# Performance work log

Measured on AMD Instinct MI355X. Metric: run time of the kernel, lower is better.

The kernel has to match this reference:

```python
import jax, jax.numpy as jnp
import numpy as np

DM, NEXPERTS, SETS, ESIZE = 1024, 32, 4, 32
B, S = 2, 8192


def setup_inputs() -> dict:
    key = jax.random.key(0)
    ks = jax.random.split(key, 7)
    sc = 0.02
    return {
        "x": jax.random.normal(ks[0], (B, S, DM), jnp.float32),
        "Wc": jax.random.normal(ks[1], (DM, NEXPERTS, SETS), jnp.float32) * sc,
        "bc": jax.random.normal(ks[2], (NEXPERTS, SETS), jnp.float32) * sc,
        "W1": jax.random.normal(ks[3], (NEXPERTS, SETS, DM, ESIZE), jnp.float32) * sc,
        "b1": jax.random.normal(ks[4], (NEXPERTS, SETS, ESIZE), jnp.float32) * sc,
        "W2": jax.random.normal(ks[5], (NEXPERTS, SETS, DM, ESIZE), jnp.float32) * sc,
        "b2": jax.random.normal(ks[6], (NEXPERTS, SETS, DM), jnp.float32) * sc,
    }


def reference(x, Wc, bc, W1, b1, W2, b2):
    b, s, d = x.shape
    g = Wc.shape[1]          # nexperts (= tokens per group)
    # group tokens: [..., (n g), d] -> [..., n, g, d]
    grouped = x.reshape(b, s // g, g, d)
    # controller logits: [b, n, t, e, s]
    logits = jnp.einsum('bntd,des->bntes', grouped, Wc) + bc
    # tie-breaker varying along the token axis (dim -3)
    tie = jnp.linspace(0.0, 1e-6, g, dtype=x.dtype).reshape(-1, 1, 1)
    logits = logits + tie
    # hard one-hot permutation: argmax over tokens per (expert, set)
    perm = (logits == jnp.max(logits, axis=-3, keepdims=True)).astype(x.dtype)
    # dispatch: [b, n, e, s, d]
    permuted = jnp.einsum('bntd,bntes->bnesd', grouped, perm)
    # per-(expert,set) MLP
    inner = jax.nn.relu(jnp.einsum('bnesd,esdf->bnesf', permuted, W1) + b1)
    result_permuted = jnp.einsum('bnesf,esdf->bnesd', inner, W2) + b2
    # combine back to tokens: [b, n, t, d]
    result = jnp.einsum('bnesd,bntes->bntd', result_permuted, perm)
    return result.reshape(b, s, d)
```

## Files before the change

### kernel.cpp

```cpp
#include <hip/hip_runtime.h>
#include <hip/hip_bf16.h>

#define DM   1024
#define NES  128
#define GT   32
#define NGRP 512
#define FSZ  32
#define MARGIN_EPS 1e-3f

typedef float f32x4 __attribute__((ext_vector_type(4)));
typedef short s16x8 __attribute__((ext_vector_type(8)));

__device__ inline unsigned short f2bf(float f) {
  union { float f; unsigned int u; } x; x.f = f;
  unsigned int r = x.u + 0x7fffu + ((x.u >> 16) & 1u);
  return (unsigned short)(r >> 16);
}
__device__ inline float bf2f(unsigned short h) {
  union { unsigned int u; float f; } x; x.u = ((unsigned int)h) << 16;
  return x.f;
}

__global__ __launch_bounds__(256) void kSplit(const float* __restrict__ x,
                                              unsigned short* __restrict__ xh,
                                              unsigned short* __restrict__ xl) {
  size_t i = ((size_t)blockIdx.x * 256 + threadIdx.x) * 8;
  float4 a = *(const float4*)&x[i];
  float4 b = *(const float4*)&x[i + 4];
  float v[8] = {a.x, a.y, a.z, a.w, b.x, b.y, b.z, b.w};
  s16x8 h, lo;
#pragma unroll
  for (int k = 0; k < 8; ++k) {
    unsigned short hh = f2bf(v[k]);
    h[k]  = (short)hh;
    lo[k] = (short)f2bf(v[k] - bf2f(hh));
  }
  *(s16x8*)&xh[i] = h;
  *(s16x8*)&xl[i] = lo;
}

__global__ __launch_bounds__(256) void kW(const float* __restrict__ W1,
                                          const float* __restrict__ W2,
                                          const float* __restrict__ Wc,
                                          unsigned short* __restrict__ W1f,
                                          unsigned short* __restrict__ W2f,
                                          unsigned short* __restrict__ Wchf,
                                          unsigned short* __restrict__ Wclf) {
  const int bid = blockIdx.x;
  if (bid < 2048) {
    int idx = bid * 256 + threadIdx.x;
    int l = idx & 63, nh = (idx >> 6) & 1, kt = (idx >> 7) & 31, es = idx >> 12;
    const float* src = W1 + ((size_t)es * DM + kt * 32 + (l >> 4) * 8) * FSZ
                          + nh * 16 + (l & 15);
    s16x8 v;
#pragma unroll
    for (int i = 0; i < 8; ++i) v[i] = (short)f2bf(src[(size_t)i * FSZ]);
    *(s16x8*)(W1f + (size_t)idx * 8) = v;
  } else if (bid < 4096) {
    int idx = (bid - 2048) * 256 + threadIdx.x;
    int l = idx & 63, dt = (idx >> 6) & 63, es = idx >> 12;
    const float* src = W2 + ((size_t)es * DM + dt * 16 + (l & 15)) * FSZ + (l >> 4) * 8;
    float4 a = *(const float4*)src;
    float4 b = *(const float4*)(src + 4);
    s16x8 v;
    v[0] = (short)f2bf(a.x); v[1] = (short)f2bf(a.y);
    v[2] = (short)f2bf(a.z); v[3] = (short)f2bf(a.w);
    v[4] = (short)f2bf(b.x); v[5] = (short)f2bf(b.y);
    v[6] = (short)f2bf(b.z); v[7] = (short)f2bf(b.w);
    *(s16x8*)(W2f + (size_t)idx * 8) = v;
  } else {
    int idx = (bid - 4096) * 256 + threadIdx.x;
    int l = idx & 63, nt = (idx >> 6) & 7, kt = idx >> 9;
    const float* src = Wc + (size_t)(kt * 32 + (l >> 4) * 8) * NES + nt * 16 + (l & 15);
    s16x8 h, lo;
#pragma unroll
    for (int i = 0; i < 8; ++i) {
      float v = src[(size_t)i * NES];
      unsigned short hh = f2bf(v);
      h[i]  = (short)hh;
      lo[i] = (short)f2bf(v - bf2f(hh));
    }
    *(s16x8*)(Wchf + (size_t)idx * 8) = h;
    *(s16x8*)(Wclf + (size_t)idx * 8) = lo;
  }
}

__global__ __launch_bounds__(256, 2) void kLg(const unsigned short* __restrict__ xh,
                                              const unsigned short* __restrict__ xl,
                                              const unsigned short* __restrict__ Wchf,
                                              const unsigned short* __restrict__ Wclf,
                                              const float* __restrict__ bc,
                                              unsigned int* __restrict__ sel,
                                              unsigned int* __restrict__ flags,
                                              unsigned int* __restrict__ cnt) {
  __shared__ float lg[GT * NES];
  const int g   = blockIdx.x;
  const int tid = threadIdx.x;
  const int l   = tid & 63, w = tid >> 6;
  const int r15 = l & 15, q = l >> 4;

  const unsigned short* ah0 = xh + ((size_t)g * GT + r15) * DM + q * 8;
  const unsigned short* ah1 = ah0 + 16 * DM;
  const unsigned short* al0 = xl + ((size_t)g * GT + r15) * DM + q * 8;
  const unsigned short* al1 = al0 + 16 * DM;

  f32x4 acc[2][2];
#pragma unroll
  for (int i = 0; i < 2; ++i)
#pragma unroll
    for (int j = 0; j < 2; ++j) acc[i][j] = (f32x4){0.f, 0.f, 0.f, 0.f};

  for (int kt = 0; kt < 32; ++kt) {
    s16x8 Ah0 = *(const s16x8*)(ah0 + kt * 32);
    s16x8 Ah1 = *(const s16x8*)(ah1 + kt * 32);
    s16x8 Al0 = *(const s16x8*)(al0 + kt * 32);
    s16x8 Al1 = *(const s16x8*)(al1 + kt * 32);
    const size_t boff = (((size_t)kt * 8 + w * 2) * 64 + l) * 8;
    s16x8 Bh0 = *(const s16x8*)(Wchf + boff);
    s16x8 Bh1 = *(const s16x8*)(Wchf + boff + 64 * 8);
    s16x8 Bl0 = *(const s16x8*)(Wclf + boff);
    s16x8 Bl1 = *(const s16x8*)(Wclf + boff + 64 * 8);
    acc[0][0] = __builtin_amdgcn_mfma_f32_16x16x32_bf16(Ah0, Bh0, acc[0][0], 0, 0, 0);
    acc[0][0] = __builtin_amdgcn_mfma_f32_16x16x32_bf16(Al0, Bh0, acc[0][0], 0, 0, 0);
    acc[0][0] = __builtin_amdgcn_mfma_f32_16x16x32_bf16(Ah0, Bl0, acc[0][0], 0, 0, 0);
    acc[0][1] = __builtin_amdgcn_mfma_f32_16x16x32_bf16(Ah0, Bh1, acc[0][1], 0, 0, 0);
    acc[0][1] = __builtin_amdgcn_mfma_f32_16x16x32_bf16(Al0, Bh1, acc[0][1], 0, 0, 0);
    acc[0][1] = __builtin_amdgcn_mfma_f32_16x16x32_bf16(Ah0, Bl1, acc[0][1], 0, 0, 0);
    acc[1][0] = __builtin_amdgcn_mfma_f32_16x16x32_bf16(Ah1, Bh0, acc[1][0], 0, 0, 0);
    acc[1][0] = __builtin_amdgcn_mfma_f32_16x16x32_bf16(Al1, Bh0, acc[1][0], 0, 0, 0);
    acc[1][0] = __builtin_amdgcn_mfma_f32_16x16x32_bf16(Ah1, Bl0, acc[1][0], 0, 0, 0);
    acc[1][1] = __builtin_amdgcn_mfma_f32_16x16x32_bf16(Ah1, Bh1, acc[1][1], 0, 0, 0);
    acc[1][1] = __builtin_amdgcn_mfma_f32_16x16x32_bf16(Al1, Bh1, acc[1][1], 0, 0, 0);
    acc[1][1] = __builtin_amdgcn_mfma_f32_16x16x32_bf16(Ah1, Bl1, acc[1][1], 0, 0, 0);
  }

#pragma unroll
  for (int mi = 0; mi < 2; ++mi)
#pragma unroll
    for (int ni = 0; ni < 2; ++ni)
#pragma unroll
      for (int r = 0; r < 4; ++r) {
        int t  = mi * 16 + q * 4 + r;
        int es = w * 32 + ni * 16 + r15;
        lg[t * NES + es] = acc[mi][ni][r];
      }
  __syncthreads();

  if (tid < NES) {
    const int es = tid;
    const float bce = bc[es];
    float m1 = -INFINITY, m2 = -INFINITY;
    int am = 0;
    for (int t = 0; t < GT; ++t) {
      float v = (lg[t * NES + es] + bce) + (float)((double)t * (1e-6 / 31.0));
      if (v > m1) { m2 = m1; m1 = v; am = t; }
      else if (v > m2) m2 = v;
    }
    sel[(size_t)g * NES + es] = 1u << am;
    if (!(m1 - m2 > MARGIN_EPS)) {
      unsigned int p = atomicAdd(cnt, 1u);
      flags[p] = ((unsigned int)g << 7) | (unsigned int)es;
    }
  }
}

__global__ __launch_bounds__(64) void kFix(const float* __restrict__ x,
                                           const float* __restrict__ Wc,
                                           const float* __restrict__ bc,
                                           unsigned int* __restrict__ sel,
                                           const unsigned int* __restrict__ flags,
                                           const unsigned int* __restrict__ cnt) {
  __shared__ float v[GT];
  const int tid = threadIdx.x;
  const unsigned int n = *cnt;
  for (unsigned int i = blockIdx.x; i < n; i += gridDim.x) {
    const unsigned int f = flags[i];
    const int g = (int)(f >> 7), es = (int)(f & 127u);
    if (tid < GT) {
      const float* xr = x + ((size_t)g * GT + tid) * DM;
      const float* wcol = Wc + es;
      float acc = 0.f;
      for (int c = 0; c < 16; ++c) {
        float part = 0.f;
#pragma unroll 4
        for (int s = 0; s < 16; ++s) {
          const int d0 = c * 64 + s * 4;
          float4 xv = *(const float4*)&xr[d0];
          float w0 = wcol[(size_t)(d0 + 0) * NES];
          float w1 = wcol[(size_t)(d0 + 1) * NES];
          float w2 = wcol[(size_t)(d0 + 2) * NES];
          float w3 = wcol[(size_t)(d0 + 3) * NES];
          part = fmaf(xv.x, w0, part);
          part = fmaf(xv.y, w1, part);
          part = fmaf(xv.z, w2, part);
          part = fmaf(xv.w, w3, part);
        }
        acc += part;
      }
      v[tid] = (acc + bc[es]) + (float)((double)tid * (1e-6 / 31.0));
    }
    __syncthreads();
    if (tid == 0) {
      float m = -INFINITY;
      for (int t = 0; t < GT; ++t) m = fmaxf(m, v[t]);
      unsigned int msk = 0u;
      for (int t = 0; t < GT; ++t) if (v[t] == m) msk |= (1u << t);
      sel[(size_t)g * NES + es] = msk;
    }
    __syncthreads();
  }
}

__global__ __launch_bounds__(256, 2) void kBm(const unsigned short* __restrict__ xb,
                                              const unsigned short* __restrict__ W1f,
                                              const float* __restrict__ b1,
                                              const unsigned int* __restrict__ sel,
                                              unsigned short* __restrict__ innerb) {
  __shared__ unsigned short As[128 * 128];
  __shared__ int tokL[128];
  __shared__ unsigned int mulL[128];
  const int bid = blockIdx.x;
  const int es = bid >> 2, g0 = (bid & 3) * 128;
  const int tid = threadIdx.x;
  const int l = tid & 63, w = tid >> 6;
  const int r15 = l & 15, q = l >> 4;
  const int mw = w * 32;

  if (tid < 128) {
    unsigned int m = sel[(size_t)(g0 + tid) * NES + es];
    tokL[tid] = (g0 + tid) * GT + (__ffs(m) - 1);
    mulL[tid] = (m & (m - 1)) ? m : 0u;
  }

  const int r = tid >> 1, p = tid & 1;
  const int swz = (r & 7) << 4;
  const unsigned int dbase = (unsigned int)r * 256 + (unsigned int)p * 128;

  f32x4 acc[2][2];
#pragma unroll
  for (int i = 0; i < 2; ++i)
#pragma unroll
    for (int j = 0; j < 2; ++j) acc[i][j] = (f32x4){0.f, 0.f, 0.f, 0.f};

  for (int c = 0; c < 8; ++c) {
    __syncthreads();
    unsigned int mm = mulL[r];
    if (!mm) {
      const unsigned short* src = xb + (size_t)tokL[r] * DM + c * 128 + p * 64;
#pragma unroll
      for (int j = 0; j < 8; ++j) {
        s16x8 v = *(const s16x8*)(src + j * 8);
        *(s16x8*)((char*)As + ((dbase + j * 16) ^ swz)) = v;
      }
    } else {
      size_t grow = (size_t)(g0 + r) * GT;
#pragma unroll
      for (int j = 0; j < 8; ++j) {
        float av[8] = {0.f, 0.f, 0.f, 0.f, 0.f, 0.f, 0.f, 0.f};
        unsigned int m2 = mm;
        while (m2) {
          int tt = __ffs(m2) - 1; m2 &= m2 - 1;
          s16x8 v = *(const s16x8*)(xb + (grow + tt) * DM + c * 128 + p * 64 + j * 8);
#pragma unroll
          for (int k = 0; k < 8; ++k) av[k] += bf2f((unsigned short)v[k]);
        }
        s16x8 o;
#pragma unroll
        for (int k = 0; k < 8; ++k) o[k] = (short)f2bf(av[k]);
        *(s16x8*)((char*)As + ((dbase + j * 16) ^ swz)) = o;
      }
    }
    __syncthreads();

#pragma unroll
    for (int s = 0; s < 4; ++s) {
      const int ks = c * 4 + s;
      const unsigned short* bp = W1f + ((size_t)es * 32 + ks) * 1024 + l * 8;
      s16x8 bf0 = *(const s16x8*)bp;
      s16x8 bf1 = *(const s16x8*)(bp + 512);
      const int row0 = mw + r15, row1 = mw + 16 + r15;
      s16x8 a0 = *(const s16x8*)((char*)As +
                   (((unsigned)row0 * 256 + s * 64 + q * 16) ^ ((row0 & 7) << 4)));
      s16x8 a1 = *(const s16x8*)((char*)As +
                   (((unsigned)row1 * 256 + s * 64 + q * 16) ^ ((row1 & 7) << 4)));
      acc[0][0] = __builtin_amdgcn_mfma_f32_16x16x32_bf16(a0, bf0, acc[0][0], 0, 0, 0);
      acc[0][1] = __builtin_amdgcn_mfma_f32_16x16x32_bf16(a0, bf1, acc[0][1], 0, 0, 0);
      acc[1][0] = __builtin_amdgcn_mfma_f32_16x16x32_bf16(a1, bf0, acc[1][0], 0, 0, 0);
      acc[1][1] = __builtin_amdgcn_mfma_f32_16x16x32_bf16(a1, bf1, acc[1][1], 0, 0, 0);
    }
  }

  float bia0 = b1[es * FSZ + r15];
  float bia1 = b1[es * FSZ + 16 + r15];
#pragma unroll
  for (int i = 0; i < 2; ++i)
#pragma unroll
    for (int rr = 0; rr < 4; ++rr) {
      int g = g0 + mw + i * 16 + q * 4 + rr;
      unsigned short* op = innerb + ((size_t)es * NGRP + g) * FSZ;
      op[r15]      = f2bf(fmaxf(acc[i][0][rr] + bia0, 0.f));
      op[16 + r15] = f2bf(fmaxf(acc[i][1][rr] + bia1, 0.f));
    }
}

__global__ __launch_bounds__(256) void kC1(const unsigned short* __restrict__ innerb,
                                           const unsigned short* __restrict__ W2f,
                                           const float* __restrict__ b2,
                                           unsigned short* __restrict__ Rb,
                                           int es0, int Ec) {
  const int bid = blockIdx.x;
  const int esl = bid >> 5;
  const int es  = es0 + esl;
  const int mt  = (bid >> 3) & 3;
  const int nt  = bid & 7;
  const int tid = threadIdx.x;
  const int l = tid & 63, w = tid >> 6;
  const int r15 = l & 15, q = l >> 4;
  const int g0 = mt * 128 + (w >> 1) * 64;
  const int n0 = nt * 128 + (w & 1) * 64;

  const unsigned short* Ab = innerb + ((size_t)es * NGRP + g0 + r15) * FSZ + q * 8;
  const unsigned short* Bb = W2f + (((size_t)es * 64 + (n0 >> 4)) * 64 + l) * 8;
  s16x8 a[4], b[4];
#pragma unroll
  for (int i = 0; i < 4; ++i) a[i] = *(const s16x8*)(Ab + (size_t)i * 16 * FSZ);
#pragma unroll
  for (int j = 0; j < 4; ++j) b[j] = *(const s16x8*)(Bb + (size_t)j * 64 * 8);

  const f32x4 z = {0.f, 0.f, 0.f, 0.f};
  f32x4 acc[4][4];
#pragma unroll
  for (int i = 0; i < 4; ++i)
#pragma unroll
    for (int j = 0; j < 4; ++j)
      acc[i][j] = __builtin_amdgcn_mfma_f32_16x16x32_bf16(a[i], b[j], z, 0, 0, 0);

#pragma unroll
  for (int j = 0; j < 4; ++j) {
    const int col = n0 + j * 16 + r15;
    const float b2v = b2[(size_t)es * DM + col];
#pragma unroll
    for (int i = 0; i < 4; ++i) {
#pragma unroll
      for (int r = 0; r < 4; ++r) {
        const int g = g0 + i * 16 + q * 4 + r;
        Rb[((size_t)g * Ec + esl) * DM + col] = f2bf(acc[i][j][r] + b2v);
      }
    }
  }
}

__global__ __launch_bounds__(256) void kC2(const unsigned short* __restrict__ Rb,
                                           const unsigned int* __restrict__ sel,
                                           float* __restrict__ out,
                                           int es0, int Ec, int direct) {
  __shared__ unsigned int cnt[32];
  __shared__ unsigned char list[32][128];
  const int bid = blockIdx.x;
  const int g = bid >> 2, dq = bid & 3;
  const int tid = threadIdx.x;
  if (tid < 32) cnt[tid] = 0;
  __syncthreads();
  if (tid < Ec) {
    unsigned int m = sel[(size_t)g * NES + es0 + tid];
    while (m) { int t = __ffs(m) - 1; m &= m - 1;
      unsigned int p = atomicAdd(&cnt[t], 1u);
      list[t][p] = (unsigned char)tid; }
  }
  __syncthreads();
  const int t = tid >> 3, part = tid & 7;
  const int d0 = dq * 256 + part * 32;
  const int n = (int)cnt[t];
  const unsigned short* base = Rb + (size_t)g * Ec * DM + d0;

  float acc[32];
#pragma unroll
  for (int i = 0; i < 32; ++i) acc[i] = 0.f;

  s16x8 cur[4];
  if (n) {
    const unsigned short* r = base + (size_t)list[t][0] * DM;
#pragma unroll
    for (int v = 0; v < 4; ++v) cur[v] = *(const s16x8*)(r + v * 8);
  }
  for (int e = 0; e < n; ++e) {
    s16x8 nxt[4];
    const bool more = (e + 1 < n);
    if (more) {
      const unsigned short* r = base + (size_t)list[t][e + 1] * DM;
#pragma unroll
      for (int v = 0; v < 4; ++v) nxt[v] = *(const s16x8*)(r + v * 8);
    }
#pragma unroll
    for (int v = 0; v < 4; ++v)
#pragma unroll
      for (int k = 0; k < 8; ++k)
        acc[v * 8 + k] += bf2f((unsigned short)cur[v][k]);
    if (more) {
#pragma unroll
      for (int v = 0; v < 4; ++v) cur[v] = nxt[v];
    }
  }

  float* op = out + ((size_t)g * GT + t) * DM + d0;
  if (direct) {
#pragma unroll
    for (int v = 0; v < 8; ++v)
      *(float4*)&op[v * 4] =
          make_float4(acc[v * 4], acc[v * 4 + 1], acc[v * 4 + 2], acc[v * 4 + 3]);
  } else {
#pragma unroll
    for (int v = 0; v < 8; ++v) {
      float4 o = *(float4*)&op[v * 4];
      o.x += acc[v * 4]; o.y += acc[v * 4 + 1];
      o.z += acc[v * 4 + 2]; o.w += acc[v * 4 + 3];
      *(float4*)&op[v * 4] = o;
    }
  }
}

extern "C" void kernel_launch(void* const* d_in, const int* in_sizes, int n_in,
                              void* d_out, int out_size, void* d_ws, size_t ws_size,
                              hipStream_t stream) {
  const float* x  = (const float*)d_in[0];
  const float* Wc = (const float*)d_in[1];
  const float* bc = (const float*)d_in[2];
  const float* W1 = (const float*)d_in[3];
  const float* b1 = (const float*)d_in[4];
  const float* W2 = (const float*)d_in[5];
  const float* b2 = (const float*)d_in[6];
  float* out = (float*)d_out;

  unsigned int* sel    = (unsigned int*)d_ws;
  unsigned int* flags  = (unsigned int*)((char*)d_ws + (256u << 10));
  unsigned int* cntr   = (unsigned int*)((char*)d_ws + (512u << 10));
  unsigned short* Wchf = (unsigned short*)((char*)d_ws + (768u << 10));
  unsigned short* Wclf = (unsigned short*)((char*)d_ws + (1u << 20));
  unsigned short* innerb = (unsigned short*)((char*)d_ws + (2u << 20));
  unsigned short* W2f  = (unsigned short*)((char*)d_ws + (6u << 20));
  unsigned short* W1f  = (unsigned short*)((char*)d_ws + (15u << 20));
  unsigned short* xb   = (unsigned short*)((char*)d_ws + (24u << 20));
  unsigned short* xl   = (unsigned short*)((char*)d_ws + (60u << 20));
  unsigned short* Rb   = (unsigned short*)((char*)d_ws + (15u << 20));

  int Ec = 128;
  while (Ec > 1 && (15u << 20) + (size_t)NGRP * Ec * DM * 2 > ws_size) Ec >>= 1;
  const int NC = NES / Ec;

  hipMemsetAsync(cntr, 0, 4, stream);
  if (NC > 1)
    hipMemsetAsync(d_out, 0, (size_t)out_size * sizeof(float), stream);
  kSplit<<<8192, 256, 0, stream>>>(x, xb, xl);
  kW<<<4160, 256, 0, stream>>>(W1, W2, Wc, W1f, W2f, Wchf, Wclf);
  kLg<<<NGRP, 256, 0, stream>>>(xb, xl, Wchf, Wclf, bc, sel, flags, cntr);
  kFix<<<1024, 64, 0, stream>>>(x, Wc, bc, sel, flags, cntr);
  kBm<<<NGRP, 256, 0, stream>>>(xb, W1f, b1, sel, innerb);
  for (int c = 0; c < NC; ++c) {
    kC1<<<Ec * 32, 256, 0, stream>>>(innerb, W2f, b2, Rb, c * Ec, Ec);
    kC2<<<NGRP * 4, 256, 0, stream>>>(Rb, sel, out, c * Ec, Ec, NC == 1);
  }
}
```

Before: 239.2 us.

## Fuse bf16 hi/lo split of x into controller logits kernel

Removes the separate kSplit kernel and performs the bf16 hi/lo split of x inside kLg, reading fp32 x directly. The low part is never written to memory, and only one wave group writes the high part that kBm consumes later. kLg moves to 512 threads with 8 waves, each owning one 16-token half and a 32-column slice, which spreads the MFMA work across more waves. This drops a full write and re-read of the lo buffer and one kernel launch. In exchange, the fp32 x rows are reloaded and re-split redundantly by the four waves that share each token half.

```diff
diff --git a/kernel.cpp b/kernel.cpp
--- a/kernel.cpp
+++ b/kernel.cpp
@@ -19,24 +19,6 @@
 __device__ inline float bf2f(unsigned short h) {
   union { unsigned int u; float f; } x; x.u = ((unsigned int)h) << 16;
   return x.f;
-}
-
-__global__ __launch_bounds__(256) void kSplit(const float* __restrict__ x,
-                                              unsigned short* __restrict__ xh,
-                                              unsigned short* __restrict__ xl) {
-  size_t i = ((size_t)blockIdx.x * 256 + threadIdx.x) * 8;
-  float4 a = *(const float4*)&x[i];
-  float4 b = *(const float4*)&x[i + 4];
-  float v[8] = {a.x, a.y, a.z, a.w, b.x, b.y, b.z, b.w};
-  s16x8 h, lo;
-#pragma unroll
-  for (int k = 0; k < 8; ++k) {
-    unsigned short hh = f2bf(v[k]);
-    h[k]  = (short)hh;
-    lo[k] = (short)f2bf(v[k] - bf2f(hh));
-  }
-  *(s16x8*)&xh[i] = h;
-  *(s16x8*)&xl[i] = lo;
 }
 
 __global__ __launch_bounds__(256) void kW(const float* __restrict__ W1,
@@ -85,11 +67,11 @@
   }
 }
 
-__global__ __launch_bounds__(256, 2) void kLg(const unsigned short* __restrict__ xh,
-                                              const unsigned short* __restrict__ xl,
+__global__ __launch_bounds__(512, 4) void kLg(const float* __restrict__ x,
                                               const unsigned short* __restrict__ Wchf,
                                               const unsigned short* __restrict__ Wclf,
                                               const float* __restrict__ bc,
+                                              unsigned short* __restrict__ xh,
                                               unsigned int* __restrict__ sel,
                                               unsigned int* __restrict__ flags,
                                               unsigned int* __restrict__ cnt) {
@@ -97,53 +79,46 @@
   const int g   = blockIdx.x;
   const int tid = threadIdx.x;
   const int l   = tid & 63, w = tid >> 6;
+  const int wt  = w & 1, we = w >> 1;
   const int r15 = l & 15, q = l >> 4;
-
-  const unsigned short* ah0 = xh + ((size_t)g * GT + r15) * DM + q * 8;
-  const unsigned short* ah1 = ah0 + 16 * DM;
-  const unsigned short* al0 = xl + ((size_t)g * GT + r15) * DM + q * 8;
-  const unsigned short* al1 = al0 + 16 * DM;
-
-  f32x4 acc[2][2];
-#pragma unroll
-  for (int i = 0; i < 2; ++i)
-#pragma unroll
-    for (int j = 0; j < 2; ++j) acc[i][j] = (f32x4){0.f, 0.f, 0.f, 0.f};
+  const int row = g * GT + wt * 16 + r15;
+  const float* xrow = x + (size_t)row * DM + q * 8;
+  unsigned short* xhrow = xh + (size_t)row * DM + q * 8;
+
+  f32x4 acc0 = {0.f, 0.f, 0.f, 0.f}, acc1 = {0.f, 0.f, 0.f, 0.f};
 
   for (int kt = 0; kt < 32; ++kt) {
-    s16x8 Ah0 = *(const s16x8*)(ah0 + kt * 32);
-    s16x8 Ah1 = *(const s16x8*)(ah1 + kt * 32);
-    s16x8 Al0 = *(const s16x8*)(al0 + kt * 32);
-    s16x8 Al1 = *(const s16x8*)(al1 + kt * 32);
-    const size_t boff = (((size_t)kt * 8 + w * 2) * 64 + l) * 8;
-    s16x8 Bh0 = *(const s16x8*)(Wchf + boff);
-    s16x8 Bh1 = *(const s16x8*)(Wchf + boff + 64 * 8);
-    s16x8 Bl0 = *(const s16x8*)(Wclf + boff);
-    s16x8 Bl1 = *(const s16x8*)(Wclf + boff + 64 * 8);
-    acc[0][0] = __builtin_amdgcn_mfma_f32_16x16x32_bf16(Ah0, Bh0, acc[0][0], 0, 0, 0);
-    acc[0][0] = __builtin_amdgcn_mfma_f32_16x16x32_bf16(Al0, Bh0, acc[0][0], 0, 0, 0);
-    acc[0][0] = __builtin_amdgcn_mfma_f32_16x16x32_bf16(Ah0, Bl0, acc[0][0], 0, 0, 0);
-    acc[0][1] = __builtin_amdgcn_mfma_f32_16x16x32_bf16(Ah0, Bh1, acc[0][1], 0, 0, 0);
-    acc[0][1] = __builtin_amdgcn_mfma_f32_16x16x32_bf16(Al0, Bh1, acc[0][1], 0, 0, 0);
-    acc[0][1] = __builtin_amdgcn_mfma_f32_16x16x32_bf16(Ah0, Bl1, acc[0][1], 0, 0, 0);
-    acc[1][0] = __builtin_amdgcn_mfma_f32_16x16x32_bf16(Ah1, Bh0, acc[1][0], 0, 0, 0);
-    acc[1][0] = __builtin_amdgcn_mfma_f32_16x16x32_bf16(Al1, Bh0, acc[1][0], 0, 0, 0);
-    acc[1][0] = __builtin_amdgcn_mfma_f32_16x16x32_bf16(Ah1, Bl0, acc[1][0], 0, 0, 0);
-    acc[1][1] = __builtin_amdgcn_mfma_f32_16x16x32_bf16(Ah1, Bh1, acc[1][1], 0, 0, 0);
-    acc[1][1] = __builtin_amdgcn_mfma_f32_16x16x32_bf16(Al1, Bh1, acc[1][1], 0, 0, 0);
-    acc[1][1] = __builtin_amdgcn_mfma_f32_16x16x32_bf16(Ah1, Bl1, acc[1][1], 0, 0, 0);
-  }
-
-#pragma unroll
-  for (int mi = 0; mi < 2; ++mi)
-#pragma unroll
-    for (int ni = 0; ni < 2; ++ni)
-#pragma unroll
-      for (int r = 0; r < 4; ++r) {
-        int t  = mi * 16 + q * 4 + r;
-        int es = w * 32 + ni * 16 + r15;
-        lg[t * NES + es] = acc[mi][ni][r];
-      }
+    float4 a = *(const float4*)(xrow + kt * 32);
+    float4 b = *(const float4*)(xrow + kt * 32 + 4);
+    float v[8] = {a.x, a.y, a.z, a.w, b.x, b.y, b.z, b.w};
+    s16x8 Ah, Al;
+#pragma unroll
+    for (int k = 0; k < 8; ++k) {
+      unsigned short h = f2bf(v[k]);
+      Ah[k] = (short)h;
+      Al[k] = (short)f2bf(v[k] - bf2f(h));
+    }
+    if (we == 0) *(s16x8*)(xhrow + kt * 32) = Ah;
+
+    const size_t b0 = (((size_t)kt * 8 + we * 2) * 64 + l) * 8;
+    s16x8 Bh0 = *(const s16x8*)(Wchf + b0);
+    s16x8 Bl0 = *(const s16x8*)(Wclf + b0);
+    s16x8 Bh1 = *(const s16x8*)(Wchf + b0 + 512);
+    s16x8 Bl1 = *(const s16x8*)(Wclf + b0 + 512);
+    acc0 = __builtin_amdgcn_mfma_f32_16x16x32_bf16(Ah, Bh0, acc0, 0, 0, 0);
+    acc0 = __builtin_amdgcn_mfma_f32_16x16x32_bf16(Al, Bh0, acc0, 0, 0, 0);
+    acc0 = __builtin_amdgcn_mfma_f32_16x16x32_bf16(Ah, Bl0, acc0, 0, 0, 0);
+    acc1 = __builtin_amdgcn_mfma_f32_16x16x32_bf16(Ah, Bh1, acc1, 0, 0, 0);
+    acc1 = __builtin_amdgcn_mfma_f32_16x16x32_bf16(Al, Bh1, acc1, 0, 0, 0);
+    acc1 = __builtin_amdgcn_mfma_f32_16x16x32_bf16(Ah, Bl1, acc1, 0, 0, 0);
+  }
+
+#pragma unroll
+  for (int r = 0; r < 4; ++r) {
+    const int t = wt * 16 + q * 4 + r;
+    lg[t * NES + we * 32 + r15]      = acc0[r];
+    lg[t * NES + we * 32 + 16 + r15] = acc1[r];
+  }
   __syncthreads();
 
   if (tid < NES) {
@@ -440,7 +415,6 @@
   unsigned short* W2f  = (unsigned short*)((char*)d_ws + (6u << 20));
   unsigned short* W1f  = (unsigned short*)((char*)d_ws + (15u << 20));
   unsigned short* xb   = (unsigned short*)((char*)d_ws + (24u << 20));
-  unsigned short* xl   = (unsigned short*)((char*)d_ws + (60u << 20));
   unsigned short* Rb   = (unsigned short*)((char*)d_ws + (15u << 20));
 
   int Ec = 128;
@@ -450,9 +424,8 @@
   hipMemsetAsync(cntr, 0, 4, stream);
   if (NC > 1)
     hipMemsetAsync(d_out, 0, (size_t)out_size * sizeof(float), stream);
-  kSplit<<<8192, 256, 0, stream>>>(x, xb, xl);
   kW<<<4160, 256, 0, stream>>>(W1, W2, Wc, W1f, W2f, Wchf, Wclf);
-  kLg<<<NGRP, 256, 0, stream>>>(xb, xl, Wchf, Wclf, bc, sel, flags, cntr);
+  kLg<<<NGRP, 512, 0, stream>>>(x, Wchf, Wclf, bc, xb, sel, flags, cntr);
   kFix<<<1024, 64, 0, stream>>>(x, Wc, bc, sel, flags, cntr);
   kBm<<<NGRP, 256, 0, stream>>>(xb, W1f, b1, sel, innerb);
   for (int c = 0; c < NC; ++c) {
```

Measured after the change: 232.7 us. 2.7% less time.
